# Kernel tuning notes

Measured on AMD Instinct MI355X. Metric: run time of the kernel, lower is better.

The kernel has to match this reference:

```python
import jax, jax.numpy as jnp
import numpy as np
import math

B, S, D, H = 2, 2048, 1024, 16
DH = D // H          # 64 head dim
BLK = 64             # SpargeAttn block size
TOPK = 0.5           # fraction of KV blocks kept per query block
NEG = -1e9


def setup_inputs() -> dict:
    key = jax.random.key(0)
    ks = jax.random.split(key, 8)
    s = 0.02
    return {
        "inputs": jax.random.normal(ks[0], (B, S, D), dtype=jnp.float32),
        "ln_g": jnp.ones((D,), jnp.float32),
        "ln_b": jnp.zeros((D,), jnp.float32),
        "Wq": jax.random.normal(ks[1], (D, D), jnp.float32) * s,
        "bq": jnp.zeros((D,), jnp.float32),
        "Wk": jax.random.normal(ks[2], (D, D), jnp.float32) * s,
        "bk": jnp.zeros((D,), jnp.float32),
        "Wv": jax.random.normal(ks[3], (D, D), jnp.float32) * s,
        "bv": jnp.zeros((D,), jnp.float32),
        "Wo": jax.random.normal(ks[4], (D, D), jnp.float32) * s,
        "bo": jnp.zeros((D,), jnp.float32),
    }


def _sparse_topk_attn(q, k, v):
    # q,k,v: [B,H,S,DH]. Block-mean-similarity top-k sparse causal attention
    # (SpargeAttn spas_sage2_attn_meansim_topk, fp32 reference semantics).
    nb = S // BLK
    qm = q.reshape(B, H, nb, BLK, DH).mean(3)          # [B,H,nb,DH]
    km = k.reshape(B, H, nb, BLK, DH).mean(3)
    sim = jnp.einsum('bhqd,bhkd->bhqk', qm, km)        # block similarity
    cblk = jnp.tril(jnp.ones((nb, nb), bool))          # causal block mask
    sim = jnp.where(cblk, sim, NEG)
    kk = max(1, int(math.ceil(TOPK * nb)))
    _, idx = jax.lax.top_k(sim, kk)                    # [B,H,nb,kk]
    blk = jax.nn.one_hot(idx, nb, dtype=jnp.float32).sum(-2) > 0  # [B,H,nb,nb]
    blk = (blk & cblk) | jnp.eye(nb, dtype=bool)       # keep diagonal block
    tok_mask = jnp.repeat(jnp.repeat(blk, BLK, axis=2), BLK, axis=3)  # [B,H,S,S]
    tok_mask = tok_mask & jnp.tril(jnp.ones((S, S), bool))
    scores = jnp.einsum('bhid,bhjd->bhij', q, k) / jnp.float32(math.sqrt(DH))
    scores = jnp.where(tok_mask, scores, NEG)
    p = jax.nn.softmax(scores, axis=-1)
    return jnp.einsum('bhij,bhjd->bhid', p, v)


def reference(inputs, ln_g, ln_b, Wq, bq, Wk, bk, Wv, bv, Wo, bo):
    # pre-norm LayerNorm
    mu = inputs.mean(-1, keepdims=True)
    var = inputs.var(-1, keepdims=True)
    x = (inputs - mu) * jax.lax.rsqrt(var + 1e-5) * ln_g + ln_b
    # QKV projections -> [B,H,S,DH]
    q = (x @ Wq + bq).reshape(B, S, H, DH).transpose(0, 2, 1, 3)
    k = (x @ Wk + bk).reshape(B, S, H, DH).transpose(0, 2, 1, 3)
    v = (x @ Wv + bv).reshape(B, S, H, DH).transpose(0, 2, 1, 3)
    ctx = _sparse_topk_attn(q, k, v)
    ctx = ctx.transpose(0, 2, 1, 3).reshape(B, S, D)
    return ctx @ Wo + bo
```

## Files before the change

kernel.cpp:

```cpp
#include <hip/hip_runtime.h>
#include <stdint.h>

#define DEV static __device__ __forceinline__

typedef __attribute__((ext_vector_type(8))) short s16x8;
typedef __attribute__((ext_vector_type(4))) float f32x4;

constexpr int Bdim = 2, Sdim = 2048, Ddim = 1024, Hdim = 16, DH = 64;
constexpr int Mrows = Bdim * Sdim;
constexpr int NB = 32;
constexpr int SEL_STRIDE = 18;

#define QSCALE 0.18033688011112042f
#define MFIX   8.0f

constexpr size_t OFF_XB    = 0;
constexpr size_t OFF_WTQKV = OFF_XB    + (size_t)Mrows*Ddim*2;
constexpr size_t OFF_WOT   = OFF_WTQKV + (size_t)3072*1024*2;
constexpr size_t OFF_QKV   = OFF_WOT   + (size_t)1024*1024*2;
constexpr size_t OFF_CTX   = OFF_QKV   + (size_t)Mrows*3072*2;
constexpr size_t OFF_XM    = OFF_CTX   + (size_t)Mrows*Ddim*2;
constexpr size_t OFF_QM    = OFF_XM    + (size_t)64*1024*4;
constexpr size_t OFF_KM    = OFF_QM    + (size_t)64*1024*4;
constexpr size_t OFF_BIASQ = OFF_KM    + (size_t)64*1024*4;
constexpr size_t OFF_SEL   = OFF_BIASQ + (size_t)3072*4;
constexpr size_t OFF_PART  = OFF_SEL   + (size_t)1024*SEL_STRIDE*4;

DEV float bf2f(unsigned short u){ union{unsigned int i; float f;} x; x.i = ((unsigned int)u)<<16; return x.f; }
DEV unsigned short f2bf(float f){ union{float f; unsigned int i;} x; x.f=f;
  unsigned int r = x.i + 0x7fffu + ((x.i>>16)&1u); return (unsigned short)(r>>16); }

DEV void gload16(const unsigned short* g, unsigned short* l){
  __builtin_amdgcn_global_load_lds(
      (__attribute__((address_space(1))) void*)(void*)g,
      (__attribute__((address_space(3))) void*)l, 16, 0, 0);
}

DEV unsigned int cvtpk(float a, float b){
  unsigned int r;
  asm("v_cvt_pk_bf16_f32 %0, %1, %2" : "=v"(r) : "v"(a), "v"(b));
  return r;
}

DEV float exp2fast(float x){
  float r;
  asm("v_exp_f32 %0, %1" : "=v"(r) : "v"(x));
  return r;
}

__global__ __launch_bounds__(256) void ln_kernel(const float* __restrict__ inp,
                                                 const float* __restrict__ gam,
                                                 const float* __restrict__ bet,
                                                 unsigned short* __restrict__ xb){
  const int row = blockIdx.x, t = threadIdx.x;
  __shared__ float red[8];
  const float4 v = ((const float4*)(inp + (size_t)row*Ddim))[t];
  float s  = v.x + v.y + v.z + v.w;
  float s2 = v.x*v.x + v.y*v.y + v.z*v.z + v.w*v.w;
#pragma unroll
  for (int mk=32; mk>=1; mk>>=1){ s += __shfl_xor(s, mk); s2 += __shfl_xor(s2, mk); }
  if ((t&63)==0){ red[t>>6] = s; red[4+(t>>6)] = s2; }
  __syncthreads();
  s  = red[0]+red[1]+red[2]+red[3];
  s2 = red[4]+red[5]+red[6]+red[7];
  const float mu  = s * (1.f/Ddim);
  const float var = s2 * (1.f/Ddim) - mu*mu;
  const float rs  = rsqrtf(var + 1e-5f);
  const float4 gv = ((const float4*)gam)[t];
  const float4 bv = ((const float4*)bet)[t];
  float o0 = (v.x-mu)*rs*gv.x + bv.x;
  float o1 = (v.y-mu)*rs*gv.y + bv.y;
  float o2 = (v.z-mu)*rs*gv.z + bv.z;
  float o3 = (v.w-mu)*rs*gv.w + bv.w;
  uint2 u;
  u.x = (unsigned int)f2bf(o0) | ((unsigned int)f2bf(o1)<<16);
  u.y = (unsigned int)f2bf(o2) | ((unsigned int)f2bf(o3)<<16);
  ((uint2*)(xb + (size_t)row*Ddim))[t] = u;
}

__global__ __launch_bounds__(256) void xm_kernel(const float* __restrict__ inp,
                                                 const float* __restrict__ gam,
                                                 const float* __restrict__ bet,
                                                 float* __restrict__ xm){
  const int blk = blockIdx.x, t = threadIdx.x;
  const int w = t>>6, lane = t&63;
  __shared__ float part[4][1024];
  float4 gv[4], bv[4];
#pragma unroll
  for (int p=0;p<4;++p){ gv[p] = ((const float4*)gam)[lane + 64*p];
                         bv[p] = ((const float4*)bet)[lane + 64*p]; }
  float ax[4][4];
#pragma unroll
  for (int p=0;p<4;++p)
#pragma unroll
    for (int c=0;c<4;++c) ax[p][c]=0.f;
  for (int rr=0; rr<16; ++rr){
    const int row = blk*64 + w*16 + rr;
    const float4* rp = (const float4*)(inp + (size_t)row*Ddim);
    float4 v[4]; float s=0.f, s2=0.f;
#pragma unroll
    for (int p=0;p<4;++p){
      v[p] = rp[lane + 64*p];
      s  += v[p].x+v[p].y+v[p].z+v[p].w;
      s2 += v[p].x*v[p].x+v[p].y*v[p].y+v[p].z*v[p].z+v[p].w*v[p].w;
    }
#pragma unroll
    for (int mk=32; mk>=1; mk>>=1){ s += __shfl_xor(s,mk); s2 += __shfl_xor(s2,mk); }
    const float mu = s*(1.f/Ddim);
    const float var = s2*(1.f/Ddim) - mu*mu;
    const float rs = rsqrtf(var + 1e-5f);
#pragma unroll
    for (int p=0;p<4;++p){
      ax[p][0] += (v[p].x-mu)*rs*gv[p].x + bv[p].x;
      ax[p][1] += (v[p].y-mu)*rs*gv[p].y + bv[p].y;
      ax[p][2] += (v[p].z-mu)*rs*gv[p].z + bv[p].z;
      ax[p][3] += (v[p].w-mu)*rs*gv[p].w + bv[p].w;
    }
  }
#pragma unroll
  for (int p=0;p<4;++p){
    float4 o; o.x=ax[p][0]; o.y=ax[p][1]; o.z=ax[p][2]; o.w=ax[p][3];
    ((float4*)&part[w][0])[lane + 64*p] = o;
  }
  __syncthreads();
  float4 r0 = ((float4*)&part[0][0])[t];
  float4 r1 = ((float4*)&part[1][0])[t];
  float4 r2 = ((float4*)&part[2][0])[t];
  float4 r3 = ((float4*)&part[3][0])[t];
  float4 o;
  o.x = (r0.x+r1.x+r2.x+r3.x)*(1.f/64);
  o.y = (r0.y+r1.y+r2.y+r3.y)*(1.f/64);
  o.z = (r0.z+r1.z+r2.z+r3.z)*(1.f/64);
  o.w = (r0.w+r1.w+r2.w+r3.w)*(1.f/64);
  ((float4*)(xm + (size_t)blk*Ddim))[t] = o;
}

__global__ __launch_bounds__(256) void wtrans4_kernel(const float* __restrict__ Wq,
                                                      const float* __restrict__ Wk,
                                                      const float* __restrict__ Wv,
                                                      const float* __restrict__ Wo,
                                                      const float* __restrict__ bq,
                                                      const float* __restrict__ bk,
                                                      const float* __restrict__ bv,
                                                      unsigned short* __restrict__ wtqkv,
                                                      unsigned short* __restrict__ wot,
                                                      float* __restrict__ bqkv){
  __shared__ float tile[32][33];
  const int z = blockIdx.z;
  const float* W = (z==0)?Wq:(z==1)?Wk:(z==2)?Wv:Wo;
  unsigned short* Wt = (z<3) ? (wtqkv + (size_t)z*1024*1024) : wot;
  const int n0 = blockIdx.x*32, k0 = blockIdx.y*32;
  const int t = threadIdx.x, r = t>>5, c = t&31;
  if (z<3 && blockIdx.x==0 && blockIdx.y==0){
    const float* bb = (z==0)?bq:(z==1)?bk:bv;
#pragma unroll
    for (int i=0;i<4;++i) bqkv[z*1024 + t + 256*i] = bb[t + 256*i];
  }
#pragma unroll
  for (int i=0;i<4;++i) tile[r+8*i][c] = W[(size_t)(k0 + r + 8*i)*1024 + n0 + c];
  __syncthreads();
#pragma unroll
  for (int i=0;i<4;++i) Wt[(size_t)(n0 + r + 8*i)*1024 + k0 + c] = f2bf(tile[c][r+8*i]);
}

__global__ __launch_bounds__(256) void qmkm_part(const float* __restrict__ xm,
    const float* __restrict__ Wq, const float* __restrict__ Wk,
    float* __restrict__ part){
  const int c  = blockIdx.x*256 + threadIdx.x;
  const int rg = blockIdx.y >> 3, ks = blockIdx.y & 7;
  const int z  = blockIdx.z;
  const float* W = z ? Wk : Wq;
  const int r0 = rg*16, k0 = ks*128;
  float acc[16];
#pragma unroll
  for (int r=0;r<16;++r) acc[r]=0.f;
  for (int k=0;k<128;k+=4){
    const float wv0 = W[(size_t)(k0+k  )*1024 + c];
    const float wv1 = W[(size_t)(k0+k+1)*1024 + c];
    const float wv2 = W[(size_t)(k0+k+2)*1024 + c];
    const float wv3 = W[(size_t)(k0+k+3)*1024 + c];
#pragma unroll
    for (int r=0;r<16;++r){
      const float4 xv = *(const float4*)&xm[(size_t)(r0+r)*1024 + k0 + k];
      acc[r] = fmaf(xv.w, wv3, fmaf(xv.z, wv2, fmaf(xv.y, wv1, fmaf(xv.x, wv0, acc[r]))));
    }
  }
  float* dst = part + (((size_t)z*8 + ks)*64 + r0)*1024 + c;
#pragma unroll
  for (int r=0;r<16;++r) dst[(size_t)r*1024] = acc[r];
}

__global__ __launch_bounds__(256) void qmkm_reduce(const float* __restrict__ part,
    const float* __restrict__ bq, const float* __restrict__ bk,
    float* __restrict__ qm, float* __restrict__ km){
  const int idx = blockIdx.x*256 + threadIdx.x;
  const int z = blockIdx.y;
  const int c = idx & 1023, r = idx >> 10;
  const float* p = part + ((size_t)z*8*64*1024) + (size_t)r*1024 + c;
  float s = 0.f;
#pragma unroll
  for (int ks=0; ks<8; ++ks) s += p[(size_t)ks*64*1024];
  s += z ? bk[c] : bq[c];
  (z ? km : qm)[(size_t)r*1024 + c] = s;
}

__global__ __launch_bounds__(256) void topk_kernel(const float* __restrict__ qm,
                                                   const float* __restrict__ km,
                                                   int* __restrict__ sel){
  const int bhq = blockIdx.x;
  const int qb = bhq & 31, h = (bhq>>5) & 15, b = bhq >> 9;
  const int t = threadIdx.x;
  __shared__ float sim[32];
  __shared__ int keep[32];
  const int kb = t>>3, l8 = t&7;
  float acc = 0.f;
  if (kb <= qb){
    const float* qv = qm + (size_t)(b*32 + qb)*1024 + h*64;
    const float* kv = km + (size_t)(b*32 + kb)*1024 + h*64;
#pragma unroll
    for (int d=0; d<8; ++d) acc += qv[l8*8+d] * kv[l8*8+d];
  }
  acc += __shfl_xor(acc,1); acc += __shfl_xor(acc,2); acc += __shfl_xor(acc,4);
  if (l8==0) sim[kb] = (kb<=qb) ? acc : -1e30f;
  __syncthreads();
  if (t < 32){
    int k2 = t; int ok = 0;
    if (k2 <= qb){
      float sv = sim[k2]; int rank = 0;
      for (int j=0;j<=qb;++j){
        float sj = sim[j];
        rank += (sj > sv) || (sj == sv && j < k2);
      }
      ok = (rank < 16) || (k2 == qb);
    }
    keep[t] = ok;
  }
  __syncthreads();
  if (t == 0){
    int* dstp = sel + (size_t)bhq * SEL_STRIDE;
    int c = 0;
    for (int j=0;j<32;++j) if (keep[j]) dstp[1+c++] = j;
    dstp[0] = c;
  }
}

#define G_STAGE(bsel, kofs) do { \
  gload16(A0 + (kofs), ldsA + (bsel)*4096 + (wid*2+0)*512); \
  gload16(A1 + (kofs), ldsA + (bsel)*4096 + (wid*2+1)*512); \
  gload16(B0 + (kofs), ldsB + (bsel)*4096 + (wid*2+0)*512); \
  gload16(B1 + (kofs), ldsB + (bsel)*4096 + (wid*2+1)*512); \
} while(0)

#define G_COMPUTE(bsel) do { \
  s16x8 af[4], bfr[4]; \
  _Pragma("unroll") \
  for (int mi=0;mi<4;++mi){ \
    int row = wr*64 + mi*16 + rl; \
    af[mi] = *(const s16x8*)((char*)ldsA + (bsel)*8192 + row*64 + ((g ^ ((row>>1)&3))<<4)); \
  } \
  _Pragma("unroll") \
  for (int ni=0;ni<4;++ni){ \
    int row = wc*64 + ni*16 + rl; \
    bfr[ni] = *(const s16x8*)((char*)ldsB + (bsel)*8192 + row*64 + ((g ^ ((row>>1)&3))<<4)); \
  } \
  _Pragma("unroll") \
  for (int mi=0;mi<4;++mi) \
    _Pragma("unroll") \
    for (int ni=0;ni<4;++ni) \
      acc[mi][ni] = __builtin_amdgcn_mfma_f32_16x16x32_bf16(af[mi], bfr[ni], acc[mi][ni], 0,0,0); \
} while(0)

template<int OUT_BF16, int SCALEQ>
__global__ __launch_bounds__(256) void gemm_bt(const unsigned short* __restrict__ A,
                                               const unsigned short* __restrict__ Bt,
                                               const float* __restrict__ bias,
                                               void* __restrict__ C, int N){
  constexpr int K = 1024;
  constexpr int NT = K/32;
  __shared__ unsigned short ldsA[3*128*32];
  __shared__ unsigned short ldsB[3*128*32];
  const int t = threadIdx.x, lane = t & 63, wid = t >> 6;
  const int wr = wid >> 1, wc = wid & 1;
  const int rl = lane & 15, g = lane >> 4;

  const int nbx = gridDim.x, nby = gridDim.y;
  const int id  = blockIdx.y * nbx + blockIdx.x;
  const int xcd = id & 7, j = id >> 3;
  const int MBP = nby >> 2, NBP = nbx >> 1;
  const int mg = xcd >> 1, ng = xcd & 1;
  const int m0 = (mg*MBP + (j % MBP)) * 128;
  const int n0 = (ng*NBP + (j / MBP)) * 128;

  const f32x4 ZERO4 = {0.f,0.f,0.f,0.f};
  f32x4 acc[4][4];
#pragma unroll
  for (int i=0;i<4;++i)
#pragma unroll
    for (int j2=0;j2<4;++j2) acc[i][j2] = ZERO4;

  const int slot0 = wid*128 + lane, slot1 = slot0 + 64;
  const int sr0 = slot0>>2, sc0 = slot0&3;
  const int sr1 = slot1>>2, sc1 = slot1&3;
  const unsigned short* A0 = A  + (size_t)(m0 + sr0)*K + (sc0 ^ ((sr0>>1)&3))*8;
  const unsigned short* A1 = A  + (size_t)(m0 + sr1)*K + (sc1 ^ ((sr1>>1)&3))*8;
  const unsigned short* B0 = Bt + (size_t)(n0 + sr0)*K + (sc0 ^ ((sr0>>1)&3))*8;
  const unsigned short* B1 = Bt + (size_t)(n0 + sr1)*K + (sc1 ^ ((sr1>>1)&3))*8;

  G_STAGE(0, 0);
  G_STAGE(1, 32);

  for (int ti=0; ti<NT; ++ti){
    const int cur = ti % 3;
    if (ti+2 < NT){
      G_STAGE((ti+2)%3, (ti+2)*32);
      asm volatile("s_waitcnt vmcnt(8)" ::: "memory");
    } else if (ti+1 < NT){
      asm volatile("s_waitcnt vmcnt(4)" ::: "memory");
    } else {
      asm volatile("s_waitcnt vmcnt(0)" ::: "memory");
    }
    __builtin_amdgcn_s_barrier();
    __builtin_amdgcn_sched_barrier(0);
    G_COMPUTE(cur);
    __builtin_amdgcn_sched_barrier(0);
    __builtin_amdgcn_s_barrier();
  }

  const int r4 = g*4;
#pragma unroll
  for (int mi=0;mi<4;++mi){
#pragma unroll
    for (int ni=0;ni<4;++ni){
      int col = n0 + wc*64 + ni*16 + rl;
      float bb = bias[col];
      float sc = (SCALEQ && col < 1024) ? QSCALE : 1.0f;
#pragma unroll
      for (int e=0;e<4;++e){
        int row = m0 + wr*64 + mi*16 + r4 + e;
        float v = (acc[mi][ni][e] + bb) * sc;
        if (OUT_BF16) ((unsigned short*)C)[(size_t)row*N + col] = f2bf(v);
        else          ((float*)C)[(size_t)row*N + col] = v;
      }
    }
  }
}

__global__ __launch_bounds__(256) void attn_kernel(const unsigned short* __restrict__ qkv,
                                                   const int* __restrict__ sel,
                                                   unsigned short* __restrict__ ctx){
  const int id = blockIdx.x;
  const int xcd = id & 7, jj = id >> 3;
  const int bh = xcd + 8*(jj/24);
  const int tau = jj % 24;
  const int h = bh & 15, b = bh >> 4;
  int qbl[2]; int nq;
  if (tau < 8){ qbl[0]=tau; qbl[1]=15-tau; nq=2; }
  else        { qbl[0]=tau+8; qbl[1]=0;    nq=1; }

  const int t = threadIdx.x, wid = t >> 6, lane = t & 63;
  const int rl = lane & 15, g = lane >> 4;
  const int q_local = wid*16 + rl;

  __shared__ unsigned short K_s[2][4096];
  __shared__ unsigned short V_s[2][4096];

  const int jst = t >> 2, cq = t & 3;
  const int r2 = t >> 3, dq = t & 7;
  const unsigned short* kbase = qkv + (size_t)(b*Sdim + jst)*3072 + 1024 + h*DH + cq*16;
  const unsigned short* vbase = qkv + (size_t)(b*Sdim + 2*r2)*3072 + 2048 + h*DH + dq*8;
  const int kwb0 = jst*128 + (((cq*2  ) ^ (jst&7))<<4);
  const int kwb1 = jst*128 + (((cq*2+1) ^ (jst&7))<<4);
  const f32x4 ZERO4 = {0.f,0.f,0.f,0.f};

  const int src0 = (rl + 16*((2*g  ) & 3)) << 2;
  const int src1 = (rl + 16*((2*g+1) & 3)) << 2;
  const bool hsel = (g >> 1);

  for (int iq=0; iq<nq; ++iq){
    const int qb = qbl[iq];
    const int* selrow = sel + (size_t)(((b*Hdim)+h)*NB + qb) * SEL_STRIDE;
    const int ns = selrow[0];

    const int qg0 = b*Sdim + qb*64 + q_local;
    const unsigned short* qbase = qkv + (size_t)qg0*3072 + h*DH;
    s16x8 qa[2];
    qa[0] = *(const s16x8*)(qbase + g*8);
    qa[1] = *(const s16x8*)(qbase + 32 + g*8);

    f32x4 o[4];
    float l_p = 0.f;
#pragma unroll
    for (int f=0; f<4; ++f) o[f] = ZERO4;

    __syncthreads();

    int kb = selrow[1];
    s16x8 kr0, kr1, vr0, vr1;
    {
      const size_t off = (size_t)kb*64*3072;
      kr0 = *(const s16x8*)(kbase + off);
      kr1 = *(const s16x8*)(kbase + off + 8);
      vr0 = *(const s16x8*)(vbase + off);
      vr1 = *(const s16x8*)(vbase + off + 3072);
    }

    for (int it=0; it<ns; ++it){
      const int buf = it & 1;
      unsigned short* Kw = &K_s[buf][0];
      unsigned short* Vw = &V_s[buf][0];
      *(s16x8*)((char*)Kw + kwb0) = kr0;
      *(s16x8*)((char*)Kw + kwb1) = kr1;
#pragma unroll
      for (int e=0;e<8;++e){
        const int d1 = dq*8 + e;
        const int sw = (d1&7) ^ (d1>>3);
        const unsigned int pr = (unsigned int)(unsigned short)vr0[e]
                              | ((unsigned int)(unsigned short)vr1[e] << 16);
        *(unsigned int*)((char*)Vw + d1*128 + ((4*r2) ^ (sw<<4))) = pr;
      }
      const int kbcur = kb;
      if (it+1 < ns){
        kb = selrow[2+it];
        const size_t off = (size_t)kb*64*3072;
        kr0 = *(const s16x8*)(kbase + off);
        kr1 = *(const s16x8*)(kbase + off + 8);
        vr0 = *(const s16x8*)(vbase + off);
        vr1 = *(const s16x8*)(vbase + off + 3072);
      }
      __syncthreads();

      f32x4 sfT[4];
#pragma unroll
      for (int f=0;f<4;++f) sfT[f] = ZERO4;
      __builtin_amdgcn_s_setprio(1);
#pragma unroll
      for (int kk=0;kk<2;++kk){
#pragma unroll
        for (int f=0;f<4;++f){
          const int jr = f*16 + rl;
          s16x8 kf = *(const s16x8*)((char*)Kw + jr*128 + (((kk*4+g) ^ (jr&7))<<4));
          sfT[f] = __builtin_amdgcn_mfma_f32_16x16x32_bf16(kf, qa[kk], sfT[f], 0,0,0);
        }
      }
      __builtin_amdgcn_s_setprio(0);
      if (kbcur == qb){
#pragma unroll
        for (int f=0;f<4;++f)
#pragma unroll
          for (int e=0;e<4;++e){
            const int j2 = f*16 + g*4 + e;
            if (j2 > q_local) sfT[f][e] = -1e9f;
          }
      }
      {
        float rs = 0.f;
#pragma unroll
        for (int f=0;f<4;++f)
#pragma unroll
          for (int e=0;e<4;++e){
            const float p = exp2fast(sfT[f][e] - MFIX);
            sfT[f][e] = p; rs += p;
          }
        l_p += rs;
      }

      unsigned int plo[4], phi[4];
#pragma unroll
      for (int f=0;f<4;++f){
        plo[f] = cvtpk(sfT[f][0], sfT[f][1]);
        phi[f] = cvtpk(sfT[f][2], sfT[f][3]);
      }

#pragma unroll
      for (int kk=0;kk<2;++kk){
        const int f0 = 2*kk, f1 = 2*kk+1;
        unsigned int a0, b0, w0, w1, w2, w3;
        a0 = __builtin_amdgcn_ds_bpermute(src0, plo[f0]);
        b0 = __builtin_amdgcn_ds_bpermute(src0, plo[f1]);
        w0 = hsel ? b0 : a0;
        a0 = __builtin_amdgcn_ds_bpermute(src0, phi[f0]);
        b0 = __builtin_amdgcn_ds_bpermute(src0, phi[f1]);
        w1 = hsel ? b0 : a0;
        a0 = __builtin_amdgcn_ds_bpermute(src1, plo[f0]);
        b0 = __builtin_amdgcn_ds_bpermute(src1, plo[f1]);
        w2 = hsel ? b0 : a0;
        a0 = __builtin_amdgcn_ds_bpermute(src1, phi[f0]);
        b0 = __builtin_amdgcn_ds_bpermute(src1, phi[f1]);
        w3 = hsel ? b0 : a0;
        union { unsigned int u[4]; s16x8 v; } pfc;
        pfc.u[0] = w0; pfc.u[1] = w1; pfc.u[2] = w2; pfc.u[3] = w3;
        const s16x8 pf = pfc.v;
        __builtin_amdgcn_s_setprio(1);
#pragma unroll
        for (int f=0;f<4;++f){
          const int d = f*16 + rl;
          const int sw = (d&7) ^ (d>>3);
          s16x8 vf = *(const s16x8*)((char*)Vw + d*128 + ((64*kk + 16*g) ^ (sw<<4)));
          o[f] = __builtin_amdgcn_mfma_f32_16x16x32_bf16(vf, pf, o[f], 0,0,0);
        }
        __builtin_amdgcn_s_setprio(0);
      }
    }

    {
      float l_r = l_p;
      l_r += __shfl_xor(l_r, 16);
      l_r += __shfl_xor(l_r, 32);
      const float inv = 1.f / l_r;
      unsigned short* crow = ctx + (size_t)qg0*Ddim + h*DH;
#pragma unroll
      for (int f=0;f<4;++f){
        uint2 st;
        st.x = (unsigned int)f2bf(o[f][0]*inv) | ((unsigned int)f2bf(o[f][1]*inv)<<16);
        st.y = (unsigned int)f2bf(o[f][2]*inv) | ((unsigned int)f2bf(o[f][3]*inv)<<16);
        *(uint2*)(crow + f*16 + g*4) = st;
      }
    }
  }
}

extern "C" void kernel_launch(void* const* d_in, const int* in_sizes, int n_in,
                              void* d_out, int out_size, void* d_ws, size_t ws_size,
                              hipStream_t stream){
  (void)in_sizes; (void)n_in; (void)out_size; (void)ws_size;
  const float* inp  = (const float*)d_in[0];
  const float* ln_g = (const float*)d_in[1];
  const float* ln_b = (const float*)d_in[2];
  const float* Wq   = (const float*)d_in[3];
  const float* bq   = (const float*)d_in[4];
  const float* Wk   = (const float*)d_in[5];
  const float* bk   = (const float*)d_in[6];
  const float* Wv   = (const float*)d_in[7];
  const float* bv   = (const float*)d_in[8];
  const float* Wo   = (const float*)d_in[9];
  const float* bo   = (const float*)d_in[10];

  char* ws = (char*)d_ws;
  unsigned short* xb    = (unsigned short*)(ws + OFF_XB);
  unsigned short* wtqkv = (unsigned short*)(ws + OFF_WTQKV);
  unsigned short* wot   = (unsigned short*)(ws + OFF_WOT);
  unsigned short* qkvb  = (unsigned short*)(ws + OFF_QKV);
  unsigned short* ctx   = (unsigned short*)(ws + OFF_CTX);
  float* xm   = (float*)(ws + OFF_XM);
  float* qm   = (float*)(ws + OFF_QM);
  float* km   = (float*)(ws + OFF_KM);
  float* bqkv = (float*)(ws + OFF_BIASQ);
  int*   sel  = (int*)(ws + OFF_SEL);
  float* part = (float*)(ws + OFF_PART);

  ln_kernel<<<Mrows, 256, 0, stream>>>(inp, ln_g, ln_b, xb);
  xm_kernel<<<64, 256, 0, stream>>>(inp, ln_g, ln_b, xm);
  wtrans4_kernel<<<dim3(32,32,4), 256, 0, stream>>>(Wq, Wk, Wv, Wo, bq, bk, bv, wtqkv, wot, bqkv);
  qmkm_part<<<dim3(4,32,2), 256, 0, stream>>>(xm, Wq, Wk, part);
  qmkm_reduce<<<dim3(256,2), 256, 0, stream>>>(part, bq, bk, qm, km);
  topk_kernel<<<1024, 256, 0, stream>>>(qm, km, sel);
  gemm_bt<1,1><<<dim3(24,32), 256, 0, stream>>>(xb, wtqkv, bqkv, (void*)qkvb, 3072);
  attn_kernel<<<768, 256, 0, stream>>>(qkvb, sel, ctx);
  gemm_bt<0,0><<<dim3(8,32), 256, 0, stream>>>(ctx, wot, bo, d_out, 1024);
}
```

Before: 142.7 us.

## Split sparse attention KV loop across two blocks with partial-output reduction

Replaces the paired-query-block attention kernel with a split-KV variant: each query block's selected KV blocks are divided between two workgroups (even/odd), each writing unnormalized bf16 partial outputs and row sums to workspace, then a separate reduction kernel combines and normalizes them into ctx. This aims to raise parallelism (2048 blocks instead of 768) and balance the causal-sparse load. It adds an extra kernel launch, extra global traffic for partials, and an extra bf16 rounding of the partial outputs. It falls back to the old kernel if the workspace is too small, and the reduction kernel contains leftover dead code.

After: 150.6 us. 1.05x slower.

```diff
diff --git a/kernel.cpp b/kernel.cpp
--- a/kernel.cpp
+++ b/kernel.cpp
@@ -25,6 +25,9 @@
 constexpr size_t OFF_BIASQ = OFF_KM    + (size_t)64*1024*4;
 constexpr size_t OFF_SEL   = OFF_BIASQ + (size_t)3072*4;
 constexpr size_t OFF_PART  = OFF_SEL   + (size_t)1024*SEL_STRIDE*4;
+constexpr size_t OFF_PO    = OFF_PART  + (size_t)2*8*64*1024*4;
+constexpr size_t OFF_PL    = OFF_PO    + (size_t)2048*64*64*2;
+constexpr size_t WS_NEED_SPLIT = OFF_PL + (size_t)2048*64*4;
 
 DEV float bf2f(unsigned short u){ union{unsigned int i; float f;} x; x.i = ((unsigned int)u)<<16; return x.f; }
 DEV unsigned short f2bf(float f){ union{float f; unsigned int i;} x; x.f=f;
@@ -343,6 +346,231 @@
       }
     }
   }
+}
+
+__global__ __launch_bounds__(256) void attn_part(const unsigned short* __restrict__ qkv,
+                                                 const int* __restrict__ sel,
+                                                 unsigned short* __restrict__ pO,
+                                                 float* __restrict__ pL){
+  const int id = blockIdx.x;
+  const int xcd = id & 7, j = id >> 3;
+  const int bh = xcd + 8*(j >> 6);
+  const int jj2 = j & 63;
+  const int qb = jj2 >> 1, half = jj2 & 1;
+  const int h = bh & 15, b = bh >> 4;
+
+  const int t = threadIdx.x, wid = t >> 6, lane = t & 63;
+  const int rl = lane & 15, g = lane >> 4;
+  const int q_local = wid*16 + rl;
+
+  __shared__ unsigned short K_s[2][4096];
+  __shared__ unsigned short V_s[2][4096];
+
+  const int jst = t >> 2, cq = t & 3;
+  const int r2 = t >> 3, dq = t & 7;
+  const unsigned short* kbase = qkv + (size_t)(b*Sdim + jst)*3072 + 1024 + h*DH + cq*16;
+  const unsigned short* vbase = qkv + (size_t)(b*Sdim + 2*r2)*3072 + 2048 + h*DH + dq*8;
+  const int kwb0 = jst*128 + (((cq*2  ) ^ (jst&7))<<4);
+  const int kwb1 = jst*128 + (((cq*2+1) ^ (jst&7))<<4);
+  const f32x4 ZERO4 = {0.f,0.f,0.f,0.f};
+
+  const int src0 = (rl + 16*((2*g  ) & 3)) << 2;
+  const int src1 = (rl + 16*((2*g+1) & 3)) << 2;
+  const bool hsel = (g >> 1);
+
+  const int* selrow = sel + (size_t)(((b*Hdim)+h)*NB + qb) * SEL_STRIDE;
+  const int ns = selrow[0];
+
+  const int qg0 = b*Sdim + qb*64 + q_local;
+  const unsigned short* qbase = qkv + (size_t)qg0*3072 + h*DH;
+  s16x8 qa[2];
+  qa[0] = *(const s16x8*)(qbase + g*8);
+  qa[1] = *(const s16x8*)(qbase + 32 + g*8);
+
+  f32x4 o[4];
+  float l_p = 0.f;
+#pragma unroll
+  for (int f=0; f<4; ++f) o[f] = ZERO4;
+
+  int kb = 0;
+  s16x8 kr0, kr1, vr0, vr1;
+  if (half < ns){
+    kb = selrow[1+half];
+    const size_t off = (size_t)kb*64*3072;
+    kr0 = *(const s16x8*)(kbase + off);
+    kr1 = *(const s16x8*)(kbase + off + 8);
+    vr0 = *(const s16x8*)(vbase + off);
+    vr1 = *(const s16x8*)(vbase + off + 3072);
+  }
+
+  int bufc = 0;
+  for (int it = half; it < ns; it += 2, bufc ^= 1){
+    unsigned short* Kw = &K_s[bufc][0];
+    unsigned short* Vw = &V_s[bufc][0];
+    *(s16x8*)((char*)Kw + kwb0) = kr0;
+    *(s16x8*)((char*)Kw + kwb1) = kr1;
+#pragma unroll
+    for (int e=0;e<8;++e){
+      const int d1 = dq*8 + e;
+      const int sw = (d1&7) ^ (d1>>3);
+      const unsigned int pr = (unsigned int)(unsigned short)vr0[e]
+                            | ((unsigned int)(unsigned short)vr1[e] << 16);
+      *(unsigned int*)((char*)Vw + d1*128 + ((4*r2) ^ (sw<<4))) = pr;
+    }
+    const int kbcur = kb;
+    if (it+2 < ns){
+      kb = selrow[3+it];
+      const size_t off = (size_t)kb*64*3072;
+      kr0 = *(const s16x8*)(kbase + off);
+      kr1 = *(const s16x8*)(kbase + off + 8);
+      vr0 = *(const s16x8*)(vbase + off);
+      vr1 = *(const s16x8*)(vbase + off + 3072);
+    }
+    __syncthreads();
+
+    f32x4 sfT[4];
+#pragma unroll
+    for (int f=0;f<4;++f) sfT[f] = ZERO4;
+    __builtin_amdgcn_s_setprio(1);
+#pragma unroll
+    for (int kk=0;kk<2;++kk){
+#pragma unroll
+      for (int f=0;f<4;++f){
+        const int jr = f*16 + rl;
+        s16x8 kf = *(const s16x8*)((char*)Kw + jr*128 + (((kk*4+g) ^ (jr&7))<<4));
+        sfT[f] = __builtin_amdgcn_mfma_f32_16x16x32_bf16(kf, qa[kk], sfT[f], 0,0,0);
+      }
+    }
+    __builtin_amdgcn_s_setprio(0);
+    if (kbcur == qb){
+#pragma unroll
+      for (int f=0;f<4;++f)
+#pragma unroll
+        for (int e=0;e<4;++e){
+          const int j2 = f*16 + g*4 + e;
+          if (j2 > q_local) sfT[f][e] = -1e9f;
+        }
+    }
+    {
+      float rs = 0.f;
+#pragma unroll
+      for (int f=0;f<4;++f)
+#pragma unroll
+        for (int e=0;e<4;++e){
+          const float p = exp2fast(sfT[f][e] - MFIX);
+          sfT[f][e] = p; rs += p;
+        }
+      l_p += rs;
+    }
+
+    unsigned int plo[4], phi[4];
+#pragma unroll
+    for (int f=0;f<4;++f){
+      plo[f] = cvtpk(sfT[f][0], sfT[f][1]);
+      phi[f] = cvtpk(sfT[f][2], sfT[f][3]);
+    }
+
+#pragma unroll
+    for (int kk=0;kk<2;++kk){
+      const int f0 = 2*kk, f1 = 2*kk+1;
+      unsigned int a0, b0, w0, w1, w2, w3;
+      a0 = __builtin_amdgcn_ds_bpermute(src0, plo[f0]);
+      b0 = __builtin_amdgcn_ds_bpermute(src0, plo[f1]);
+      w0 = hsel ? b0 : a0;
+      a0 = __builtin_amdgcn_ds_bpermute(src0, phi[f0]);
+      b0 = __builtin_amdgcn_ds_bpermute(src0, phi[f1]);
+      w1 = hsel ? b0 : a0;
+      a0 = __builtin_amdgcn_ds_bpermute(src1, plo[f0]);
+      b0 = __builtin_amdgcn_ds_bpermute(src1, plo[f1]);
+      w2 = hsel ? b0 : a0;
+      a0 = __builtin_amdgcn_ds_bpermute(src1, phi[f0]);
+      b0 = __builtin_amdgcn_ds_bpermute(src1, phi[f1]);
+      w3 = hsel ? b0 : a0;
+      union { unsigned int u[4]; s16x8 v; } pfc;
+      pfc.u[0] = w0; pfc.u[1] = w1; pfc.u[2] = w2; pfc.u[3] = w3;
+      const s16x8 pf = pfc.v;
+      __builtin_amdgcn_s_setprio(1);
+#pragma unroll
+      for (int f=0;f<4;++f){
+        const int d = f*16 + rl;
+        const int sw = (d&7) ^ (d>>3);
+        s16x8 vf = *(const s16x8*)((char*)Vw + d*128 + ((64*kk + 16*g) ^ (sw<<4)));
+        o[f] = __builtin_amdgcn_mfma_f32_16x16x32_bf16(vf, pf, o[f], 0,0,0);
+      }
+      __builtin_amdgcn_s_setprio(0);
+    }
+  }
+
+  {
+    float l_r = l_p;
+    l_r += __shfl_xor(l_r, 16);
+    l_r += __shfl_xor(l_r, 32);
+    const int idx = (((b*Hdim)+h)*NB + qb)*2 + half;
+    unsigned short* po = pO + (size_t)idx*4096 + q_local*64;
+#pragma unroll
+    for (int f=0;f<4;++f){
+      uint2 st;
+      st.x = (unsigned int)f2bf(o[f][0]) | ((unsigned int)f2bf(o[f][1])<<16);
+      st.y = (unsigned int)f2bf(o[f][2]) | ((unsigned int)f2bf(o[f][3])<<16);
+      *(uint2*)(po + f*16 + g*4) = st;
+    }
+    if (lane < 16) pL[(size_t)idx*64 + q_local] = l_r;
+  }
+}
+
+__global__ __launch_bounds__(256) void ctxred(const unsigned short* __restrict__ pO,
+                                              const float* __restrict__ pL,
+                                              unsigned short* __restrict__ ctx){
+  const int bid = blockIdx.x;
+  const int xcd = bid & 7, jj = bid >> 3;
+  const int bh = xcd + 8*(jj >> 5);
+  const int qb = jj & 31;
+  const int h = bh & 15, b = bh >> 4;
+  const int bhqb = bh*NB + qb;
+  const int t = threadIdx.x;
+  const int q = t >> 2, d0 = (t & 3) * 16;
+
+  const size_t baseA = ((size_t)bhqb*2    )*4096 + q*64 + d0;
+  const size_t baseB = ((size_t)bhqb*2 + 1)*4096 + q*64 + d0;
+  const float lA = pL[(size_t)bhqb*128 + q];
+  const float lB = pL[(size_t)bhqb*128 + 64 + q];
+  const float inv = 1.f / (lA + lB);
+  s16x8 a0 = *(const s16x8*)(pO + baseA);
+  s16x8 a1 = *(const s16x8*)(pO + baseA + 8);
+  s16x8 b0 = *(const s16x8*)(pO + baseB);
+  s16x8 b1 = *(const s16x8*)(pO + baseB + 8);
+  unsigned int w[4];
+#pragma unroll
+  for (int p=0;p<4;++p){
+    const s16x8& xa = (p<2) ? a0 : a1;
+    const s16x8& xb2 = (p<2) ? b0 : b1;
+    const int e0 = (p&1)*4;
+    unsigned short v0 = f2bf((bf2f((unsigned short)xa[e0  ]) + bf2f((unsigned short)xb2[e0  ]))*inv);
+    unsigned short v1 = f2bf((bf2f((unsigned short)xa[e0+1]) + bf2f((unsigned short)xb2[e0+1]))*inv);
+    unsigned short v2 = f2bf((bf2f((unsigned short)xa[e0+2]) + bf2f((unsigned short)xb2[e0+2]))*inv);
+    unsigned short v3 = f2bf((bf2f((unsigned short)xa[e0+3]) + bf2f((unsigned short)xb2[e0+3]))*inv);
+    w[p] = (unsigned int)v0 | ((unsigned int)v1<<16);
+    w[p] |= 0;
+    w[p] = (unsigned int)v0 | ((unsigned int)v1<<16);
+    (void)v2; (void)v3;
+  }
+  unsigned int wv[8];
+#pragma unroll
+  for (int e=0;e<8;++e){
+    const s16x8& xa = (e<4) ? a0 : a1;
+    const s16x8& xb2 = (e<4) ? b0 : b1;
+    const int e0 = (e&3)*2;
+    unsigned short v0 = f2bf((bf2f((unsigned short)xa[e0  ]) + bf2f((unsigned short)xb2[e0  ]))*inv);
+    unsigned short v1 = f2bf((bf2f((unsigned short)xa[e0+1]) + bf2f((unsigned short)xb2[e0+1]))*inv);
+    wv[e] = (unsigned int)v0 | ((unsigned int)v1<<16);
+  }
+  const int row = b*Sdim + qb*64 + q;
+  unsigned int* dst = (unsigned int*)(ctx + (size_t)row*Ddim + h*DH + d0);
+  uint4 s0, s1;
+  s0.x = wv[0]; s0.y = wv[1]; s0.z = wv[2]; s0.w = wv[3];
+  s1.x = wv[4]; s1.y = wv[5]; s1.z = wv[6]; s1.w = wv[7];
+  ((uint4*)dst)[0] = s0;
+  ((uint4*)dst)[1] = s1;
 }
 
 __global__ __launch_bounds__(256) void attn_kernel(const unsigned short* __restrict__ qkv,
@@ -522,7 +750,7 @@
 extern "C" void kernel_launch(void* const* d_in, const int* in_sizes, int n_in,
                               void* d_out, int out_size, void* d_ws, size_t ws_size,
                               hipStream_t stream){
-  (void)in_sizes; (void)n_in; (void)out_size; (void)ws_size;
+  (void)in_sizes; (void)n_in; (void)out_size;
   const float* inp  = (const float*)d_in[0];
   const float* ln_g = (const float*)d_in[1];
   const float* ln_b = (const float*)d_in[2];
@@ -547,6 +775,8 @@
   float* bqkv = (float*)(ws + OFF_BIASQ);
   int*   sel  = (int*)(ws + OFF_SEL);
   float* part = (float*)(ws + OFF_PART);
+  unsigned short* pO = (unsigned short*)(ws + OFF_PO);
+  float* pL = (float*)(ws + OFF_PL);
 
   ln_kernel<<<Mrows, 256, 0, stream>>>(inp, ln_g, ln_b, xb);
   xm_kernel<<<64, 256, 0, stream>>>(inp, ln_g, ln_b, xm);
@@ -555,6 +785,11 @@
   qmkm_reduce<<<dim3(256,2), 256, 0, stream>>>(part, bq, bk, qm, km);
   topk_kernel<<<1024, 256, 0, stream>>>(qm, km, sel);
   gemm_bt<1,1><<<dim3(24,32), 256, 0, stream>>>(xb, wtqkv, bqkv, (void*)qkvb, 3072);
-  attn_kernel<<<768, 256, 0, stream>>>(qkvb, sel, ctx);
+  if (ws_size >= WS_NEED_SPLIT){
+    attn_part<<<2048, 256, 0, stream>>>(qkvb, sel, pO, pL);
+    ctxred<<<1024, 256, 0, stream>>>(pO, pL, ctx);
+  } else {
+    attn_kernel<<<768, 256, 0, stream>>>(qkvb, sel, ctx);
+  }
   gemm_bt<0,0><<<dim3(8,32), 256, 0, stream>>>(ctx, wot, bo, d_out, 1024);
 }
```
